# Performance work log

Hardware: AMD Instinct MI355X
Metric: run time of the kernel (lower is better)

## Reference

```python
import jax, jax.numpy as jnp
import numpy as np

B, N, D = 4, 4096, 1024
DFF = 4 * D
K = 2048  # max(1, int(N * 0.5))


def setup_inputs() -> dict:
    key = jax.random.key(0)
    ks = jax.random.split(key, 4)
    x = jax.random.normal(ks[0], (B, N, D), dtype=jnp.float32)
    gate_w = jax.random.normal(ks[1], (1, D), dtype=jnp.float32) * 0.02
    w1 = jax.random.normal(ks[2], (D, DFF), dtype=jnp.float32) * (1.0 / np.sqrt(D))
    b1 = jnp.zeros((DFF,), dtype=jnp.float32)
    w2 = jax.random.normal(ks[3], (DFF, D), dtype=jnp.float32) * (1.0 / np.sqrt(DFF))
    b2 = jnp.zeros((D,), dtype=jnp.float32)
    return {"x": x, "gate_w": gate_w, "w1": w1, "b1": b1, "w2": w2, "b2": b2, "k": K}


def reference(x, gate_w, w1, b1, w2, b2, k):
    # scores: [B, N] = gate(x).squeeze(-1)
    scores = jnp.einsum("bnd,d->bn", x, gate_w[0])
    _, topk = jax.lax.top_k(scores, k)          # [B, k] token indices
    # gather selected tokens: [B, k, D]
    x_sel = jnp.take_along_axis(x, topk[:, :, None], axis=1)
    # ffn (d -> 4d -> d, GELU) + residual on selected tokens only
    h = jax.nn.gelu(x_sel @ w1 + b1) @ w2 + b2
    x_proc = x_sel + h
    # scatter processed tokens back into a copy of x
    b_idx = jnp.arange(x.shape[0])[:, None]      # [B, 1]
    out = x.at[b_idx, topk].set(x_proc)
    return out
```

## Files before the change

### kernel.cpp

```cpp
#include <hip/hip_runtime.h>
#include <math.h>

#define B_   4
#define N_   4096
#define D_   1024
#define DFF_ 4096
#define K_   2048

typedef __attribute__((ext_vector_type(8))) short short8;
typedef __attribute__((ext_vector_type(4))) float float4v;

__device__ __forceinline__ unsigned short f2bf(float f) {
    unsigned int u = __float_as_uint(f);
    u = (u + 0x7fffu + ((u >> 16) & 1u)) >> 16;
    return (unsigned short)u;
}

__device__ __forceinline__ void gld16(const void* g, void* l) {
    __builtin_amdgcn_global_load_lds((const __attribute__((address_space(1))) void*)g,
                                     (__attribute__((address_space(3))) void*)l, 16, 0, 0);
}

__global__ __launch_bounds__(256) void scores_kernel(const float* __restrict__ x,
                                                     const float* __restrict__ gate_w,
                                                     float* __restrict__ scores,
                                                     int* __restrict__ slot) {
    int wave = (blockIdx.x * blockDim.x + threadIdx.x) >> 6;
    int lane = threadIdx.x & 63;
    if (wave >= B_ * N_) return;
    if (lane == 1) slot[wave] = -1;
    const float4* xr = (const float4*)(x + (size_t)wave * D_);
    const float4* g  = (const float4*)gate_w;
    float acc = 0.f;
    #pragma unroll
    for (int j = 0; j < D_ / 4 / 64; ++j) {
        float4 a = xr[lane + j * 64];
        float4 b = g[lane + j * 64];
        acc += a.x * b.x + a.y * b.y + a.z * b.z + a.w * b.w;
    }
    #pragma unroll
    for (int off = 32; off > 0; off >>= 1) acc += __shfl_down(acc, off, 64);
    if (lane == 0) scores[wave] = acc;
}

__global__ __launch_bounds__(1024) void select_topk_kernel(const float* __restrict__ scores,
                                                           int* __restrict__ topk,
                                                           int* __restrict__ slot) {
    __shared__ unsigned key[N_];
    __shared__ unsigned hist[256];
    __shared__ int sh_bin, sh_rem, sh_ngt;
    __shared__ int wsum[16], woff[16];
    int b = blockIdx.x, tid = threadIdx.x;
    int lane = tid & 63, wid = tid >> 6;

    for (int i = tid; i < N_; i += 1024) {
        unsigned u = __float_as_uint(scores[b * N_ + i]);
        key[i] = (u & 0x80000000u) ? ~u : (u | 0x80000000u);
    }
    if (tid == 0) sh_ngt = 0;
    __syncthreads();

    unsigned prefix = 0, pmask = 0;
    int rem = K_;
    for (int shift = 24; shift >= 0; shift -= 8) {
        if (tid < 256) hist[tid] = 0;
        __syncthreads();
        for (int i = tid; i < N_; i += 1024) {
            unsigned k = key[i];
            if ((k & pmask) == prefix) atomicAdd(&hist[(k >> shift) & 255u], 1u);
        }
        __syncthreads();
        if (tid < 64) {
            unsigned v0 = hist[4 * lane], v1 = hist[4 * lane + 1];
            unsigned v2 = hist[4 * lane + 2], v3 = hist[4 * lane + 3];
            unsigned s3 = v3, s2 = v2 + s3, s1 = v1 + s2, s0 = v0 + s1;
            unsigned t = s0;
            #pragma unroll
            for (int off = 1; off < 64; off <<= 1) {
                unsigned u = __shfl_down(t, off, 64);
                if (lane + off < 64) t += u;
            }
            unsigned above = t - s0;
            unsigned S0 = s0 + above, S1 = s1 + above, S2 = s2 + above, S3 = s3 + above;
            unsigned R = (unsigned)rem;
            if (S0 >= R && S1 < R) { sh_bin = 4 * lane;     sh_rem = rem - (int)S1; }
            if (S1 >= R && S2 < R) { sh_bin = 4 * lane + 1; sh_rem = rem - (int)S2; }
            if (S2 >= R && S3 < R) { sh_bin = 4 * lane + 2; sh_rem = rem - (int)S3; }
            if (S3 >= R && above < R) { sh_bin = 4 * lane + 3; sh_rem = rem - (int)above; }
        }
        __syncthreads();
        prefix |= ((unsigned)sh_bin) << shift;
        pmask  |= 0xffu << shift;
        rem = sh_rem;
    }
    unsigned T = prefix;
    int c_gt = K_ - rem;

    for (int i = tid; i < N_; i += 1024) {
        bool p = key[i] > T;
        unsigned long long m = __ballot(p);
        int cnt = __popcll(m);
        int basepos = 0;
        if (lane == 0 && cnt) basepos = atomicAdd(&sh_ngt, cnt);
        basepos = __shfl(basepos, 0, 64);
        if (p) {
            int pos = basepos + __popcll(m & ((1ULL << lane) - 1ULL));
            topk[b * K_ + pos] = i;
            slot[b * N_ + i] = b * K_ + pos;
        }
    }
    int base = tid * 4, c = 0;
    #pragma unroll
    for (int j = 0; j < 4; ++j) c += (key[base + j] == T);
    int sc = c;
    #pragma unroll
    for (int off = 1; off < 64; off <<= 1) {
        int u = __shfl_up(sc, off, 64);
        if (lane >= off) sc += u;
    }
    if (lane == 63) wsum[wid] = sc;
    __syncthreads();
    if (tid == 0) {
        int run = 0;
        #pragma unroll
        for (int j = 0; j < 16; ++j) { woff[j] = run; run += wsum[j]; }
    }
    __syncthreads();
    int r = woff[wid] + sc - c;
    #pragma unroll
    for (int j = 0; j < 4; ++j) {
        if (key[base + j] == T) {
            if (r < rem) {
                topk[b * K_ + c_gt + r] = base + j;
                slot[b * N_ + base + j] = b * K_ + c_gt + r;
            }
            ++r;
        }
    }
}

__global__ __launch_bounds__(256) void gather_copy_kernel(const float* __restrict__ x,
                                                          const int* __restrict__ slot,
                                                          unsigned short* __restrict__ xsel,
                                                          float* __restrict__ out) {
    int row = blockIdx.x;
    int t = threadIdx.x;
    int s = slot[row];
    float4 v = ((const float4*)(x + (size_t)row * D_))[t];
    if (s >= 0) {
        ushort4 o;
        o.x = f2bf(v.x); o.y = f2bf(v.y); o.z = f2bf(v.z); o.w = f2bf(v.w);
        ((ushort4*)(xsel + (size_t)s * D_))[t] = o;
    } else {
        ((float4*)(out + (size_t)row * D_))[t] = v;
    }
}

__global__ __launch_bounds__(256) void transpose_both_kernel(const float* __restrict__ w1,
                                                             const float* __restrict__ w2,
                                                             unsigned short* __restrict__ w1t,
                                                             unsigned short* __restrict__ w2t) {
    __shared__ float tile[32][33];
    int bid = blockIdx.x;
    const float* src; unsigned short* dst; int R, C, bx, by;
    if (bid < 4096) { src = w1; dst = w1t; R = D_;   C = DFF_; bx = bid & 127;          by = bid >> 7; }
    else            { src = w2; dst = w2t; R = DFF_; C = D_;   bx = (bid - 4096) & 31;  by = (bid - 4096) >> 5; }
    int tx = threadIdx.x & 31, ty = threadIdx.x >> 5;
    int c = bx * 32 + tx, r0 = by * 32;
    #pragma unroll
    for (int j = ty; j < 32; j += 8) tile[j][tx] = src[(size_t)(r0 + j) * C + c];
    __syncthreads();
    int dc = by * 32 + tx, dr0 = bx * 32;
    #pragma unroll
    for (int j = ty; j < 32; j += 8) dst[(size_t)(dr0 + j) * R + dc] = f2bf(tile[tx][j]);
}


__global__ __launch_bounds__(512, 4) void ffn1_db_kernel(const unsigned short* __restrict__ A,
                                                         const unsigned short* __restrict__ Bt,
                                                         const float* __restrict__ b1,
                                                         unsigned short* __restrict__ h1) {
    constexpr int K  = D_;
    constexpr int NT = K / 32;
    __shared__ __align__(16) unsigned short smem[24576];

    const int t    = threadIdx.x;
    const int lane = t & 63;
    const int wid  = t >> 6;
    const int quad = lane >> 4;
    const int lr   = lane & 15;
    const int wr   = wid >> 1;
    const int wc   = wid & 1;
    const int row0 = blockIdx.x * 256;
    const int col0 = blockIdx.y * 128;

    const int chA0 = t, chA1 = t + 512, chB = t;
    const int rpA0 = chA0 >> 3, wA0 = (chA0 & 7) ^ (rpA0 & 7);
    const int rpA1 = chA1 >> 3, wA1 = (chA1 & 7) ^ (rpA1 & 7);
    const int rpB  = chB  >> 3, wB  = (chB  & 7) ^ (rpB  & 7);
    const char* aS0 = (const char*)A  + ((size_t)(row0 + rpA0 * 2 + (wA0 >> 2)) * K + (size_t)(wA0 & 3) * 8) * 2;
    const char* aS1 = (const char*)A  + ((size_t)(row0 + rpA1 * 2 + (wA1 >> 2)) * K + (size_t)(wA1 & 3) * 8) * 2;
    const char* bS  = (const char*)Bt + ((size_t)(col0 + rpB  * 2 + (wB  >> 2)) * K + (size_t)(wB  & 3) * 8) * 2;
    const int oA0 = chA0 * 8, oA1 = chA1 * 8, oB = 8192 + chB * 8;

    const int rbA = wr * 64 + lr, rA2 = rbA >> 1;
    const int aoff = (rA2 * 8 + ((((rbA & 1) << 2) | quad) ^ (rA2 & 7))) * 8;
    const int rbB = wc * 64 + lr, rB2 = rbB >> 1;
    const int boff = 8192 + (rB2 * 8 + ((((rbB & 1) << 2) | quad) ^ (rB2 & 7))) * 8;

    unsigned short* lds0 = smem;
    unsigned short* lds1 = smem + 12288;

    gld16(aS0, lds0 + oA0); gld16(aS1, lds0 + oA1); gld16(bS, lds0 + oB);
    aS0 += 64; aS1 += 64; bS += 64;
    asm volatile("s_waitcnt vmcnt(0)" ::: "memory");
    __builtin_amdgcn_s_barrier();

    float4v acc[4][4] = {};
    short8 af[4], bq[4];

    auto step = [&](const unsigned short* cur, unsigned short* nxt, bool pf) {
        #pragma unroll
        for (int mi = 0; mi < 4; ++mi) af[mi] = *(const short8*)(cur + aoff + mi * 512);
        #pragma unroll
        for (int ni = 0; ni < 4; ++ni) bq[ni] = *(const short8*)(cur + boff + ni * 512);
        if (pf) {
            gld16(aS0, nxt + oA0); gld16(aS1, nxt + oA1); gld16(bS, nxt + oB);
            aS0 += 64; aS1 += 64; bS += 64;
        }
        __builtin_amdgcn_sched_barrier(0);
        __builtin_amdgcn_s_setprio(1);
        #pragma unroll
        for (int mi = 0; mi < 4; ++mi)
            #pragma unroll
            for (int ni = 0; ni < 4; ++ni)
                acc[mi][ni] = __builtin_amdgcn_mfma_f32_16x16x32_bf16(af[mi], bq[ni], acc[mi][ni], 0, 0, 0);
        __builtin_amdgcn_s_setprio(0);
        asm volatile("s_waitcnt vmcnt(0)" ::: "memory");
        __builtin_amdgcn_s_barrier();
    };

    for (int kt = 0; kt < NT - 2; kt += 2) { step(lds0, lds1, true); step(lds1, lds0, true); }
    step(lds0, lds1, true);
    step(lds1, lds0, false);

    float bias[4];
    #pragma unroll
    for (int ni = 0; ni < 4; ++ni) bias[ni] = b1[col0 + wc * 64 + ni * 16 + lr];
    unsigned short* ws_ = smem + wid * 1056;
    const int ro = row0 + wr * 64, co = col0 + wc * 64;
    #pragma unroll
    for (int mi = 0; mi < 4; ++mi) {
        #pragma unroll
        for (int ni = 0; ni < 4; ++ni)
            #pragma unroll
            for (int r = 0; r < 4; ++r) {
                float u = acc[mi][ni][r] + bias[ni];
                float tt = 1.5957691216057308f * u * (1.0f + 0.044715f * u * u);
                float g = u / (1.0f + __expf(-tt));
                ws_[(quad * 4 + r) * 66 + ni * 16 + lr] = f2bf(g);
            }
        asm volatile("s_waitcnt lgkmcnt(0)" ::: "memory");
        #pragma unroll
        for (int j = 0; j < 2; ++j) {
            int chk = lane + j * 64;
            int rr = chk >> 3, cc = chk & 7;
            *(short8*)(h1 + (size_t)(ro + mi * 16 + rr) * DFF_ + co + cc * 8) =
                *(const short8*)(ws_ + rr * 66 + cc * 8);
        }
        asm volatile("s_waitcnt lgkmcnt(0)" ::: "memory");
    }
}

__global__ __launch_bounds__(256, 2) void ffn2_db_kernel(const unsigned short* __restrict__ A,
                                                         const unsigned short* __restrict__ Bt,
                                                         const float* __restrict__ b2,
                                                         const float* __restrict__ x,
                                                         const int* __restrict__ topk,
                                                         float* __restrict__ out) {
    constexpr int K  = DFF_;
    constexpr int NT = K / 32;
    __shared__ __align__(16) unsigned short smem[16384];

    const int t    = threadIdx.x;
    const int lane = t & 63;
    const int wid  = t >> 6;
    const int quad = lane >> 4;
    const int lr   = lane & 15;
    const int wr   = wid >> 1;
    const int wc   = wid & 1;
    const int row0 = blockIdx.x * 128;
    const int col0 = blockIdx.y * 128;

    const int ch0 = t, ch1 = t + 256;
    const int rp0 = ch0 >> 3, w0 = (ch0 & 7) ^ (rp0 & 7);
    const int rp1 = ch1 >> 3, w1 = (ch1 & 7) ^ (rp1 & 7);
    const char* aS0 = (const char*)A  + ((size_t)(row0 + rp0 * 2 + (w0 >> 2)) * K + (size_t)(w0 & 3) * 8) * 2;
    const char* aS1 = (const char*)A  + ((size_t)(row0 + rp1 * 2 + (w1 >> 2)) * K + (size_t)(w1 & 3) * 8) * 2;
    const char* bS0 = (const char*)Bt + ((size_t)(col0 + rp0 * 2 + (w0 >> 2)) * K + (size_t)(w0 & 3) * 8) * 2;
    const char* bS1 = (const char*)Bt + ((size_t)(col0 + rp1 * 2 + (w1 >> 2)) * K + (size_t)(w1 & 3) * 8) * 2;
    const int oA0 = ch0 * 8, oA1 = ch1 * 8;
    const int oB0 = 4096 + ch0 * 8, oB1 = 4096 + ch1 * 8;

    const int rbA = wr * 64 + lr, rA2 = rbA >> 1;
    const int aoff = (rA2 * 8 + ((((rbA & 1) << 2) | quad) ^ (rA2 & 7))) * 8;
    const int rbB = wc * 64 + lr, rB2 = rbB >> 1;
    const int boff = 4096 + (rB2 * 8 + ((((rbB & 1) << 2) | quad) ^ (rB2 & 7))) * 8;

    unsigned short* lds0 = smem;
    unsigned short* lds1 = smem + 8192;

    gld16(aS0, lds0 + oA0); gld16(aS1, lds0 + oA1);
    gld16(bS0, lds0 + oB0); gld16(bS1, lds0 + oB1);
    aS0 += 64; aS1 += 64; bS0 += 64; bS1 += 64;
    asm volatile("s_waitcnt vmcnt(0)" ::: "memory");
    __builtin_amdgcn_s_barrier();

    float4v acc[4][4] = {};
    short8 af[4], bq[4];

    auto step = [&](const unsigned short* cur, unsigned short* nxt, bool pf) {
        #pragma unroll
        for (int mi = 0; mi < 4; ++mi) af[mi] = *(const short8*)(cur + aoff + mi * 512);
        #pragma unroll
        for (int ni = 0; ni < 4; ++ni) bq[ni] = *(const short8*)(cur + boff + ni * 512);
        if (pf) {
            gld16(aS0, nxt + oA0); gld16(aS1, nxt + oA1);
            gld16(bS0, nxt + oB0); gld16(bS1, nxt + oB1);
            aS0 += 64; aS1 += 64; bS0 += 64; bS1 += 64;
        }
        __builtin_amdgcn_sched_barrier(0);
        __builtin_amdgcn_s_setprio(1);
        #pragma unroll
        for (int mi = 0; mi < 4; ++mi)
            #pragma unroll
            for (int ni = 0; ni < 4; ++ni)
                acc[mi][ni] = __builtin_amdgcn_mfma_f32_16x16x32_bf16(af[mi], bq[ni], acc[mi][ni], 0, 0, 0);
        __builtin_amdgcn_s_setprio(0);
        asm volatile("s_waitcnt vmcnt(0)" ::: "memory");
        __builtin_amdgcn_s_barrier();
    };

    for (int kt = 0; kt < NT - 2; kt += 2) { step(lds0, lds1, true); step(lds1, lds0, true); }
    step(lds0, lds1, true);
    step(lds1, lds0, false);

    #pragma unroll
    for (int mi = 0; mi < 4; ++mi) {
        #pragma unroll
        for (int r = 0; r < 4; ++r) {
            int row = row0 + wr * 64 + mi * 16 + quad * 4 + r;
            int gb = row >> 11;
            int tok = topk[row];
            size_t base = ((size_t)(gb * N_ + tok)) * D_;
            #pragma unroll
            for (int ni = 0; ni < 4; ++ni) {
                int col = col0 + wc * 64 + ni * 16 + lr;
                out[base + col] = x[base + col] + acc[mi][ni][r] + b2[col];
            }
        }
    }
}

extern "C" void kernel_launch(void* const* d_in, const int* in_sizes, int n_in,
                              void* d_out, int out_size, void* d_ws, size_t ws_size,
                              hipStream_t stream) {
    const float* x      = (const float*)d_in[0];
    const float* gate_w = (const float*)d_in[1];
    const float* w1     = (const float*)d_in[2];
    const float* b1     = (const float*)d_in[3];
    const float* w2     = (const float*)d_in[4];
    const float* b2     = (const float*)d_in[5];
    float* out = (float*)d_out;

    char* ws = (char*)d_ws;
    float*          scores = (float*)ws;
    int*            topk   = (int*)(ws + (64 << 10));
    int*            slot   = (int*)(ws + (96 << 10));
    unsigned short* xsel   = (unsigned short*)(ws + (160 << 10));
    unsigned short* w1t    = (unsigned short*)(ws + (160 << 10) + (16 << 20));
    unsigned short* w2t    = (unsigned short*)(ws + (160 << 10) + (24 << 20));
    unsigned short* h1     = (unsigned short*)(ws + (160 << 10) + (32 << 20));

    scores_kernel<<<(B_ * N_) / 4, 256, 0, stream>>>(x, gate_w, scores, slot);
    select_topk_kernel<<<B_, 1024, 0, stream>>>(scores, topk, slot);

    transpose_both_kernel<<<8192, 256, 0, stream>>>(w1, w2, w1t, w2t);

    gather_copy_kernel<<<B_ * N_, 256, 0, stream>>>(x, slot, xsel, out);

    ffn1_db_kernel<<<dim3(32, 32), 512, 0, stream>>>(xsel, w1t, b1, h1);
    ffn2_db_kernel<<<dim3(64, 8), 256, 0, stream>>>(h1, w2t, b2, x, topk, out);
}
```

Baseline: 329.8 us.

## Deepen K-step to 64 per LDS stage in both FFN GEMMs

Both FFN GEMM kernels now load 64-wide K slices per double-buffered LDS stage instead of 32, with a new row-major swizzled layout and two MFMA sub-steps per stage. This halves the number of barriers and waits per GEMM. FFN1 also drops from 512-thread 256x128 tiles to 256-thread 128x128 tiles with a doubled grid. LDS use per block grows to 64KB, which may limit occupancy.

```diff
diff --git a/kernel.cpp b/kernel.cpp
--- a/kernel.cpp
+++ b/kernel.cpp
@@ -176,111 +176,13 @@
 }
 
 
-__global__ __launch_bounds__(512, 4) void ffn1_db_kernel(const unsigned short* __restrict__ A,
-                                                         const unsigned short* __restrict__ Bt,
-                                                         const float* __restrict__ b1,
-                                                         unsigned short* __restrict__ h1) {
+__global__ __launch_bounds__(256, 2) void ffn1_k64_kernel(const unsigned short* __restrict__ A,
+                                                          const unsigned short* __restrict__ Bt,
+                                                          const float* __restrict__ b1,
+                                                          unsigned short* __restrict__ h1) {
     constexpr int K  = D_;
-    constexpr int NT = K / 32;
-    __shared__ __align__(16) unsigned short smem[24576];
-
-    const int t    = threadIdx.x;
-    const int lane = t & 63;
-    const int wid  = t >> 6;
-    const int quad = lane >> 4;
-    const int lr   = lane & 15;
-    const int wr   = wid >> 1;
-    const int wc   = wid & 1;
-    const int row0 = blockIdx.x * 256;
-    const int col0 = blockIdx.y * 128;
-
-    const int chA0 = t, chA1 = t + 512, chB = t;
-    const int rpA0 = chA0 >> 3, wA0 = (chA0 & 7) ^ (rpA0 & 7);
-    const int rpA1 = chA1 >> 3, wA1 = (chA1 & 7) ^ (rpA1 & 7);
-    const int rpB  = chB  >> 3, wB  = (chB  & 7) ^ (rpB  & 7);
-    const char* aS0 = (const char*)A  + ((size_t)(row0 + rpA0 * 2 + (wA0 >> 2)) * K + (size_t)(wA0 & 3) * 8) * 2;
-    const char* aS1 = (const char*)A  + ((size_t)(row0 + rpA1 * 2 + (wA1 >> 2)) * K + (size_t)(wA1 & 3) * 8) * 2;
-    const char* bS  = (const char*)Bt + ((size_t)(col0 + rpB  * 2 + (wB  >> 2)) * K + (size_t)(wB  & 3) * 8) * 2;
-    const int oA0 = chA0 * 8, oA1 = chA1 * 8, oB = 8192 + chB * 8;
-
-    const int rbA = wr * 64 + lr, rA2 = rbA >> 1;
-    const int aoff = (rA2 * 8 + ((((rbA & 1) << 2) | quad) ^ (rA2 & 7))) * 8;
-    const int rbB = wc * 64 + lr, rB2 = rbB >> 1;
-    const int boff = 8192 + (rB2 * 8 + ((((rbB & 1) << 2) | quad) ^ (rB2 & 7))) * 8;
-
-    unsigned short* lds0 = smem;
-    unsigned short* lds1 = smem + 12288;
-
-    gld16(aS0, lds0 + oA0); gld16(aS1, lds0 + oA1); gld16(bS, lds0 + oB);
-    aS0 += 64; aS1 += 64; bS += 64;
-    asm volatile("s_waitcnt vmcnt(0)" ::: "memory");
-    __builtin_amdgcn_s_barrier();
-
-    float4v acc[4][4] = {};
-    short8 af[4], bq[4];
-
-    auto step = [&](const unsigned short* cur, unsigned short* nxt, bool pf) {
-        #pragma unroll
-        for (int mi = 0; mi < 4; ++mi) af[mi] = *(const short8*)(cur + aoff + mi * 512);
-        #pragma unroll
-        for (int ni = 0; ni < 4; ++ni) bq[ni] = *(const short8*)(cur + boff + ni * 512);
-        if (pf) {
-            gld16(aS0, nxt + oA0); gld16(aS1, nxt + oA1); gld16(bS, nxt + oB);
-            aS0 += 64; aS1 += 64; bS += 64;
-        }
-        __builtin_amdgcn_sched_barrier(0);
-        __builtin_amdgcn_s_setprio(1);
-        #pragma unroll
-        for (int mi = 0; mi < 4; ++mi)
-            #pragma unroll
-            for (int ni = 0; ni < 4; ++ni)
-                acc[mi][ni] = __builtin_amdgcn_mfma_f32_16x16x32_bf16(af[mi], bq[ni], acc[mi][ni], 0, 0, 0);
-        __builtin_amdgcn_s_setprio(0);
-        asm volatile("s_waitcnt vmcnt(0)" ::: "memory");
-        __builtin_amdgcn_s_barrier();
-    };
-
-    for (int kt = 0; kt < NT - 2; kt += 2) { step(lds0, lds1, true); step(lds1, lds0, true); }
-    step(lds0, lds1, true);
-    step(lds1, lds0, false);
-
-    float bias[4];
-    #pragma unroll
-    for (int ni = 0; ni < 4; ++ni) bias[ni] = b1[col0 + wc * 64 + ni * 16 + lr];
-    unsigned short* ws_ = smem + wid * 1056;
-    const int ro = row0 + wr * 64, co = col0 + wc * 64;
-    #pragma unroll
-    for (int mi = 0; mi < 4; ++mi) {
-        #pragma unroll
-        for (int ni = 0; ni < 4; ++ni)
-            #pragma unroll
-            for (int r = 0; r < 4; ++r) {
-                float u = acc[mi][ni][r] + bias[ni];
-                float tt = 1.5957691216057308f * u * (1.0f + 0.044715f * u * u);
-                float g = u / (1.0f + __expf(-tt));
-                ws_[(quad * 4 + r) * 66 + ni * 16 + lr] = f2bf(g);
-            }
-        asm volatile("s_waitcnt lgkmcnt(0)" ::: "memory");
-        #pragma unroll
-        for (int j = 0; j < 2; ++j) {
-            int chk = lane + j * 64;
-            int rr = chk >> 3, cc = chk & 7;
-            *(short8*)(h1 + (size_t)(ro + mi * 16 + rr) * DFF_ + co + cc * 8) =
-                *(const short8*)(ws_ + rr * 66 + cc * 8);
-        }
-        asm volatile("s_waitcnt lgkmcnt(0)" ::: "memory");
-    }
-}
-
-__global__ __launch_bounds__(256, 2) void ffn2_db_kernel(const unsigned short* __restrict__ A,
-                                                         const unsigned short* __restrict__ Bt,
-                                                         const float* __restrict__ b2,
-                                                         const float* __restrict__ x,
-                                                         const int* __restrict__ topk,
-                                                         float* __restrict__ out) {
-    constexpr int K  = DFF_;
-    constexpr int NT = K / 32;
-    __shared__ __align__(16) unsigned short smem[16384];
+    constexpr int NT = K / 64;
+    __shared__ __align__(16) unsigned short smem[32768];
 
     const int t    = threadIdx.x;
     const int lane = t & 63;
@@ -292,44 +194,177 @@
     const int row0 = blockIdx.x * 128;
     const int col0 = blockIdx.y * 128;
 
-    const int ch0 = t, ch1 = t + 256;
-    const int rp0 = ch0 >> 3, w0 = (ch0 & 7) ^ (rp0 & 7);
-    const int rp1 = ch1 >> 3, w1 = (ch1 & 7) ^ (rp1 & 7);
-    const char* aS0 = (const char*)A  + ((size_t)(row0 + rp0 * 2 + (w0 >> 2)) * K + (size_t)(w0 & 3) * 8) * 2;
-    const char* aS1 = (const char*)A  + ((size_t)(row0 + rp1 * 2 + (w1 >> 2)) * K + (size_t)(w1 & 3) * 8) * 2;
-    const char* bS0 = (const char*)Bt + ((size_t)(col0 + rp0 * 2 + (w0 >> 2)) * K + (size_t)(w0 & 3) * 8) * 2;
-    const char* bS1 = (const char*)Bt + ((size_t)(col0 + rp1 * 2 + (w1 >> 2)) * K + (size_t)(w1 & 3) * 8) * 2;
-    const int oA0 = ch0 * 8, oA1 = ch1 * 8;
-    const int oB0 = 4096 + ch0 * 8, oB1 = 4096 + ch1 * 8;
-
-    const int rbA = wr * 64 + lr, rA2 = rbA >> 1;
-    const int aoff = (rA2 * 8 + ((((rbA & 1) << 2) | quad) ^ (rA2 & 7))) * 8;
-    const int rbB = wc * 64 + lr, rB2 = rbB >> 1;
-    const int boff = 4096 + (rB2 * 8 + ((((rbB & 1) << 2) | quad) ^ (rB2 & 7))) * 8;
+    const char* aS[4]; const char* bS[4]; int oA[4], oB[4];
+    #pragma unroll
+    for (int j = 0; j < 4; ++j) {
+        int s = t + j * 256;
+        int r = s >> 3, c = (s & 7) ^ (r & 7);
+        aS[j] = (const char*)A  + ((size_t)(row0 + r) * K + (size_t)c * 8) * 2;
+        bS[j] = (const char*)Bt + ((size_t)(col0 + r) * K + (size_t)c * 8) * 2;
+        oA[j] = s * 8;
+        oB[j] = 8192 + s * 8;
+    }
+
+    const int rbA = wr * 64 + lr;
+    const int aoff0 = (rbA * 8 + (quad       ^ (rbA & 7))) * 8;
+    const int aoff1 = (rbA * 8 + ((4 + quad) ^ (rbA & 7))) * 8;
+    const int rbB = wc * 64 + lr;
+    const int boff0 = 8192 + (rbB * 8 + (quad       ^ (rbB & 7))) * 8;
+    const int boff1 = 8192 + (rbB * 8 + ((4 + quad) ^ (rbB & 7))) * 8;
 
     unsigned short* lds0 = smem;
-    unsigned short* lds1 = smem + 8192;
-
-    gld16(aS0, lds0 + oA0); gld16(aS1, lds0 + oA1);
-    gld16(bS0, lds0 + oB0); gld16(bS1, lds0 + oB1);
-    aS0 += 64; aS1 += 64; bS0 += 64; bS1 += 64;
+    unsigned short* lds1 = smem + 16384;
+
+    #pragma unroll
+    for (int j = 0; j < 4; ++j) { gld16(aS[j], lds0 + oA[j]); gld16(bS[j], lds0 + oB[j]); }
+    #pragma unroll
+    for (int j = 0; j < 4; ++j) { aS[j] += 128; bS[j] += 128; }
     asm volatile("s_waitcnt vmcnt(0)" ::: "memory");
     __builtin_amdgcn_s_barrier();
 
     float4v acc[4][4] = {};
-    short8 af[4], bq[4];
 
     auto step = [&](const unsigned short* cur, unsigned short* nxt, bool pf) {
-        #pragma unroll
-        for (int mi = 0; mi < 4; ++mi) af[mi] = *(const short8*)(cur + aoff + mi * 512);
-        #pragma unroll
-        for (int ni = 0; ni < 4; ++ni) bq[ni] = *(const short8*)(cur + boff + ni * 512);
+        short8 af[4], bq[4];
+        #pragma unroll
+        for (int mi = 0; mi < 4; ++mi) af[mi] = *(const short8*)(cur + aoff0 + mi * 1024);
+        #pragma unroll
+        for (int ni = 0; ni < 4; ++ni) bq[ni] = *(const short8*)(cur + boff0 + ni * 1024);
         if (pf) {
-            gld16(aS0, nxt + oA0); gld16(aS1, nxt + oA1);
-            gld16(bS0, nxt + oB0); gld16(bS1, nxt + oB1);
-            aS0 += 64; aS1 += 64; bS0 += 64; bS1 += 64;
+            #pragma unroll
+            for (int j = 0; j < 4; ++j) { gld16(aS[j], nxt + oA[j]); gld16(bS[j], nxt + oB[j]); }
+            #pragma unroll
+            for (int j = 0; j < 4; ++j) { aS[j] += 128; bS[j] += 128; }
         }
         __builtin_amdgcn_sched_barrier(0);
+        __builtin_amdgcn_s_setprio(1);
+        #pragma unroll
+        for (int mi = 0; mi < 4; ++mi)
+            #pragma unroll
+            for (int ni = 0; ni < 4; ++ni)
+                acc[mi][ni] = __builtin_amdgcn_mfma_f32_16x16x32_bf16(af[mi], bq[ni], acc[mi][ni], 0, 0, 0);
+        __builtin_amdgcn_s_setprio(0);
+        #pragma unroll
+        for (int mi = 0; mi < 4; ++mi) af[mi] = *(const short8*)(cur + aoff1 + mi * 1024);
+        #pragma unroll
+        for (int ni = 0; ni < 4; ++ni) bq[ni] = *(const short8*)(cur + boff1 + ni * 1024);
+        __builtin_amdgcn_s_setprio(1);
+        #pragma unroll
+        for (int mi = 0; mi < 4; ++mi)
+            #pragma unroll
+            for (int ni = 0; ni < 4; ++ni)
+                acc[mi][ni] = __builtin_amdgcn_mfma_f32_16x16x32_bf16(af[mi], bq[ni], acc[mi][ni], 0, 0, 0);
+        __builtin_amdgcn_s_setprio(0);
+        asm volatile("s_waitcnt vmcnt(0)" ::: "memory");
+        __builtin_amdgcn_s_barrier();
+    };
+
+    for (int kt = 0; kt < NT - 2; kt += 2) { step(lds0, lds1, true); step(lds1, lds0, true); }
+    step(lds0, lds1, true);
+    step(lds1, lds0, false);
+
+    float bias[4];
+    #pragma unroll
+    for (int ni = 0; ni < 4; ++ni) bias[ni] = b1[col0 + wc * 64 + ni * 16 + lr];
+    unsigned short* ws_ = smem + wid * 1056;
+    const int ro = row0 + wr * 64, co = col0 + wc * 64;
+    #pragma unroll
+    for (int mi = 0; mi < 4; ++mi) {
+        #pragma unroll
+        for (int ni = 0; ni < 4; ++ni)
+            #pragma unroll
+            for (int r = 0; r < 4; ++r) {
+                float u = acc[mi][ni][r] + bias[ni];
+                float tt = 1.5957691216057308f * u * (1.0f + 0.044715f * u * u);
+                float g = u / (1.0f + __expf(-tt));
+                ws_[(quad * 4 + r) * 66 + ni * 16 + lr] = f2bf(g);
+            }
+        asm volatile("s_waitcnt lgkmcnt(0)" ::: "memory");
+        #pragma unroll
+        for (int j = 0; j < 2; ++j) {
+            int chk = lane + j * 64;
+            int rr = chk >> 3, cc = chk & 7;
+            *(short8*)(h1 + (size_t)(ro + mi * 16 + rr) * DFF_ + co + cc * 8) =
+                *(const short8*)(ws_ + rr * 66 + cc * 8);
+        }
+        asm volatile("s_waitcnt lgkmcnt(0)" ::: "memory");
+    }
+}
+
+__global__ __launch_bounds__(256, 2) void ffn2_k64_kernel(const unsigned short* __restrict__ A,
+                                                          const unsigned short* __restrict__ Bt,
+                                                          const float* __restrict__ b2,
+                                                          const float* __restrict__ x,
+                                                          const int* __restrict__ topk,
+                                                          float* __restrict__ out) {
+    constexpr int K  = DFF_;
+    constexpr int NT = K / 64;
+    __shared__ __align__(16) unsigned short smem[32768];
+
+    const int t    = threadIdx.x;
+    const int lane = t & 63;
+    const int wid  = t >> 6;
+    const int quad = lane >> 4;
+    const int lr   = lane & 15;
+    const int wr   = wid >> 1;
+    const int wc   = wid & 1;
+    const int row0 = blockIdx.x * 128;
+    const int col0 = blockIdx.y * 128;
+
+    const char* aS[4]; const char* bS[4]; int oA[4], oB[4];
+    #pragma unroll
+    for (int j = 0; j < 4; ++j) {
+        int s = t + j * 256;
+        int r = s >> 3, c = (s & 7) ^ (r & 7);
+        aS[j] = (const char*)A  + ((size_t)(row0 + r) * K + (size_t)c * 8) * 2;
+        bS[j] = (const char*)Bt + ((size_t)(col0 + r) * K + (size_t)c * 8) * 2;
+        oA[j] = s * 8;
+        oB[j] = 8192 + s * 8;
+    }
+
+    const int rbA = wr * 64 + lr;
+    const int aoff0 = (rbA * 8 + (quad       ^ (rbA & 7))) * 8;
+    const int aoff1 = (rbA * 8 + ((4 + quad) ^ (rbA & 7))) * 8;
+    const int rbB = wc * 64 + lr;
+    const int boff0 = 8192 + (rbB * 8 + (quad       ^ (rbB & 7))) * 8;
+    const int boff1 = 8192 + (rbB * 8 + ((4 + quad) ^ (rbB & 7))) * 8;
+
+    unsigned short* lds0 = smem;
+    unsigned short* lds1 = smem + 16384;
+
+    #pragma unroll
+    for (int j = 0; j < 4; ++j) { gld16(aS[j], lds0 + oA[j]); gld16(bS[j], lds0 + oB[j]); }
+    #pragma unroll
+    for (int j = 0; j < 4; ++j) { aS[j] += 128; bS[j] += 128; }
+    asm volatile("s_waitcnt vmcnt(0)" ::: "memory");
+    __builtin_amdgcn_s_barrier();
+
+    float4v acc[4][4] = {};
+
+    auto step = [&](const unsigned short* cur, unsigned short* nxt, bool pf) {
+        short8 af[4], bq[4];
+        #pragma unroll
+        for (int mi = 0; mi < 4; ++mi) af[mi] = *(const short8*)(cur + aoff0 + mi * 1024);
+        #pragma unroll
+        for (int ni = 0; ni < 4; ++ni) bq[ni] = *(const short8*)(cur + boff0 + ni * 1024);
+        if (pf) {
+            #pragma unroll
+            for (int j = 0; j < 4; ++j) { gld16(aS[j], nxt + oA[j]); gld16(bS[j], nxt + oB[j]); }
+            #pragma unroll
+            for (int j = 0; j < 4; ++j) { aS[j] += 128; bS[j] += 128; }
+        }
+        __builtin_amdgcn_sched_barrier(0);
+        __builtin_amdgcn_s_setprio(1);
+        #pragma unroll
+        for (int mi = 0; mi < 4; ++mi)
+            #pragma unroll
+            for (int ni = 0; ni < 4; ++ni)
+                acc[mi][ni] = __builtin_amdgcn_mfma_f32_16x16x32_bf16(af[mi], bq[ni], acc[mi][ni], 0, 0, 0);
+        __builtin_amdgcn_s_setprio(0);
+        #pragma unroll
+        for (int mi = 0; mi < 4; ++mi) af[mi] = *(const short8*)(cur + aoff1 + mi * 1024);
+        #pragma unroll
+        for (int ni = 0; ni < 4; ++ni) bq[ni] = *(const short8*)(cur + boff1 + ni * 1024);
         __builtin_amdgcn_s_setprio(1);
         #pragma unroll
         for (int mi = 0; mi < 4; ++mi)
@@ -389,6 +424,6 @@
 
     gather_copy_kernel<<<B_ * N_, 256, 0, stream>>>(x, slot, xsel, out);
 
-    ffn1_db_kernel<<<dim3(32, 32), 512, 0, stream>>>(xsel, w1t, b1, h1);
-    ffn2_db_kernel<<<dim3(64, 8), 256, 0, stream>>>(h1, w2t, b2, x, topk, out);
-}
+    ffn1_k64_kernel<<<dim3(64, 32), 256, 0, stream>>>(xsel, w1t, b1, h1);
+    ffn2_k64_kernel<<<dim3(64, 8), 256, 0, stream>>>(h1, w2t, b2, x, topk, out);
+}
```

Result: faster. 317.9 us (-3.6%).

## Replace double-buffered GEMM loops with four-stage LDS ring and partial waits

Applied to the files above, without the earlier changes.

Both FFN GEMM kernels now use a four-slot LDS ring that keeps three K-tiles of global-to-LDS loads in flight, waiting only for the oldest tile with a counted vmcnt instead of draining all loads every step. The first GEMM also moves from 256x128 tiles with 512 threads to 128x128 tiles with 256 threads, doubling its grid. The aim is to hide global memory latency behind the MFMA work. In exchange each block uses 64KB of LDS, which may reduce how many blocks fit per CU, and the smaller ffn1 tile loads operands more often.

```diff
diff --git a/kernel.cpp b/kernel.cpp
--- a/kernel.cpp
+++ b/kernel.cpp
@@ -176,111 +176,14 @@
 }
 
 
-__global__ __launch_bounds__(512, 4) void ffn1_db_kernel(const unsigned short* __restrict__ A,
-                                                         const unsigned short* __restrict__ Bt,
-                                                         const float* __restrict__ b1,
-                                                         unsigned short* __restrict__ h1) {
+
+__global__ __launch_bounds__(256, 2) void ffn1_ring_kernel(const unsigned short* __restrict__ A,
+                                                           const unsigned short* __restrict__ Bt,
+                                                           const float* __restrict__ b1,
+                                                           unsigned short* __restrict__ h1) {
     constexpr int K  = D_;
     constexpr int NT = K / 32;
-    __shared__ __align__(16) unsigned short smem[24576];
-
-    const int t    = threadIdx.x;
-    const int lane = t & 63;
-    const int wid  = t >> 6;
-    const int quad = lane >> 4;
-    const int lr   = lane & 15;
-    const int wr   = wid >> 1;
-    const int wc   = wid & 1;
-    const int row0 = blockIdx.x * 256;
-    const int col0 = blockIdx.y * 128;
-
-    const int chA0 = t, chA1 = t + 512, chB = t;
-    const int rpA0 = chA0 >> 3, wA0 = (chA0 & 7) ^ (rpA0 & 7);
-    const int rpA1 = chA1 >> 3, wA1 = (chA1 & 7) ^ (rpA1 & 7);
-    const int rpB  = chB  >> 3, wB  = (chB  & 7) ^ (rpB  & 7);
-    const char* aS0 = (const char*)A  + ((size_t)(row0 + rpA0 * 2 + (wA0 >> 2)) * K + (size_t)(wA0 & 3) * 8) * 2;
-    const char* aS1 = (const char*)A  + ((size_t)(row0 + rpA1 * 2 + (wA1 >> 2)) * K + (size_t)(wA1 & 3) * 8) * 2;
-    const char* bS  = (const char*)Bt + ((size_t)(col0 + rpB  * 2 + (wB  >> 2)) * K + (size_t)(wB  & 3) * 8) * 2;
-    const int oA0 = chA0 * 8, oA1 = chA1 * 8, oB = 8192 + chB * 8;
-
-    const int rbA = wr * 64 + lr, rA2 = rbA >> 1;
-    const int aoff = (rA2 * 8 + ((((rbA & 1) << 2) | quad) ^ (rA2 & 7))) * 8;
-    const int rbB = wc * 64 + lr, rB2 = rbB >> 1;
-    const int boff = 8192 + (rB2 * 8 + ((((rbB & 1) << 2) | quad) ^ (rB2 & 7))) * 8;
-
-    unsigned short* lds0 = smem;
-    unsigned short* lds1 = smem + 12288;
-
-    gld16(aS0, lds0 + oA0); gld16(aS1, lds0 + oA1); gld16(bS, lds0 + oB);
-    aS0 += 64; aS1 += 64; bS += 64;
-    asm volatile("s_waitcnt vmcnt(0)" ::: "memory");
-    __builtin_amdgcn_s_barrier();
-
-    float4v acc[4][4] = {};
-    short8 af[4], bq[4];
-
-    auto step = [&](const unsigned short* cur, unsigned short* nxt, bool pf) {
-        #pragma unroll
-        for (int mi = 0; mi < 4; ++mi) af[mi] = *(const short8*)(cur + aoff + mi * 512);
-        #pragma unroll
-        for (int ni = 0; ni < 4; ++ni) bq[ni] = *(const short8*)(cur + boff + ni * 512);
-        if (pf) {
-            gld16(aS0, nxt + oA0); gld16(aS1, nxt + oA1); gld16(bS, nxt + oB);
-            aS0 += 64; aS1 += 64; bS += 64;
-        }
-        __builtin_amdgcn_sched_barrier(0);
-        __builtin_amdgcn_s_setprio(1);
-        #pragma unroll
-        for (int mi = 0; mi < 4; ++mi)
-            #pragma unroll
-            for (int ni = 0; ni < 4; ++ni)
-                acc[mi][ni] = __builtin_amdgcn_mfma_f32_16x16x32_bf16(af[mi], bq[ni], acc[mi][ni], 0, 0, 0);
-        __builtin_amdgcn_s_setprio(0);
-        asm volatile("s_waitcnt vmcnt(0)" ::: "memory");
-        __builtin_amdgcn_s_barrier();
-    };
-
-    for (int kt = 0; kt < NT - 2; kt += 2) { step(lds0, lds1, true); step(lds1, lds0, true); }
-    step(lds0, lds1, true);
-    step(lds1, lds0, false);
-
-    float bias[4];
-    #pragma unroll
-    for (int ni = 0; ni < 4; ++ni) bias[ni] = b1[col0 + wc * 64 + ni * 16 + lr];
-    unsigned short* ws_ = smem + wid * 1056;
-    const int ro = row0 + wr * 64, co = col0 + wc * 64;
-    #pragma unroll
-    for (int mi = 0; mi < 4; ++mi) {
-        #pragma unroll
-        for (int ni = 0; ni < 4; ++ni)
-            #pragma unroll
-            for (int r = 0; r < 4; ++r) {
-                float u = acc[mi][ni][r] + bias[ni];
-                float tt = 1.5957691216057308f * u * (1.0f + 0.044715f * u * u);
-                float g = u / (1.0f + __expf(-tt));
-                ws_[(quad * 4 + r) * 66 + ni * 16 + lr] = f2bf(g);
-            }
-        asm volatile("s_waitcnt lgkmcnt(0)" ::: "memory");
-        #pragma unroll
-        for (int j = 0; j < 2; ++j) {
-            int chk = lane + j * 64;
-            int rr = chk >> 3, cc = chk & 7;
-            *(short8*)(h1 + (size_t)(ro + mi * 16 + rr) * DFF_ + co + cc * 8) =
-                *(const short8*)(ws_ + rr * 66 + cc * 8);
-        }
-        asm volatile("s_waitcnt lgkmcnt(0)" ::: "memory");
-    }
-}
-
-__global__ __launch_bounds__(256, 2) void ffn2_db_kernel(const unsigned short* __restrict__ A,
-                                                         const unsigned short* __restrict__ Bt,
-                                                         const float* __restrict__ b2,
-                                                         const float* __restrict__ x,
-                                                         const int* __restrict__ topk,
-                                                         float* __restrict__ out) {
-    constexpr int K  = DFF_;
-    constexpr int NT = K / 32;
-    __shared__ __align__(16) unsigned short smem[16384];
+    __shared__ __align__(16) unsigned short smem[32768];
 
     const int t    = threadIdx.x;
     const int lane = t & 63;
@@ -292,42 +195,50 @@
     const int row0 = blockIdx.x * 128;
     const int col0 = blockIdx.y * 128;
 
-    const int ch0 = t, ch1 = t + 256;
-    const int rp0 = ch0 >> 3, w0 = (ch0 & 7) ^ (rp0 & 7);
-    const int rp1 = ch1 >> 3, w1 = (ch1 & 7) ^ (rp1 & 7);
-    const char* aS0 = (const char*)A  + ((size_t)(row0 + rp0 * 2 + (w0 >> 2)) * K + (size_t)(w0 & 3) * 8) * 2;
-    const char* aS1 = (const char*)A  + ((size_t)(row0 + rp1 * 2 + (w1 >> 2)) * K + (size_t)(w1 & 3) * 8) * 2;
-    const char* bS0 = (const char*)Bt + ((size_t)(col0 + rp0 * 2 + (w0 >> 2)) * K + (size_t)(w0 & 3) * 8) * 2;
-    const char* bS1 = (const char*)Bt + ((size_t)(col0 + rp1 * 2 + (w1 >> 2)) * K + (size_t)(w1 & 3) * 8) * 2;
-    const int oA0 = ch0 * 8, oA1 = ch1 * 8;
-    const int oB0 = 4096 + ch0 * 8, oB1 = 4096 + ch1 * 8;
+    const char* aS[2]; const char* bS[2]; int oA[2], oB[2];
+    #pragma unroll
+    for (int j = 0; j < 2; ++j) {
+        int s = t + j * 256;
+        int rp = s >> 3, w = (s & 7) ^ (rp & 7);
+        int gr = rp * 2 + (w >> 2), gc = w & 3;
+        aS[j] = (const char*)A  + ((size_t)(row0 + gr) * K + (size_t)gc * 8) * 2;
+        bS[j] = (const char*)Bt + ((size_t)(col0 + gr) * K + (size_t)gc * 8) * 2;
+        oA[j] = s * 8;
+        oB[j] = 4096 + s * 8;
+    }
 
     const int rbA = wr * 64 + lr, rA2 = rbA >> 1;
     const int aoff = (rA2 * 8 + ((((rbA & 1) << 2) | quad) ^ (rA2 & 7))) * 8;
     const int rbB = wc * 64 + lr, rB2 = rbB >> 1;
     const int boff = 4096 + (rB2 * 8 + ((((rbB & 1) << 2) | quad) ^ (rB2 & 7))) * 8;
 
-    unsigned short* lds0 = smem;
-    unsigned short* lds1 = smem + 8192;
-
-    gld16(aS0, lds0 + oA0); gld16(aS1, lds0 + oA1);
-    gld16(bS0, lds0 + oB0); gld16(bS1, lds0 + oB1);
-    aS0 += 64; aS1 += 64; bS0 += 64; bS1 += 64;
-    asm volatile("s_waitcnt vmcnt(0)" ::: "memory");
+    #pragma unroll
+    for (int pt = 0; pt < 3; ++pt) {
+        unsigned short* buf = smem + pt * 8192;
+        #pragma unroll
+        for (int j = 0; j < 2; ++j) { gld16(aS[j], buf + oA[j]); gld16(bS[j], buf + oB[j]); }
+        #pragma unroll
+        for (int j = 0; j < 2; ++j) { aS[j] += 64; bS[j] += 64; }
+    }
+    asm volatile("s_waitcnt vmcnt(8)" ::: "memory");
     __builtin_amdgcn_s_barrier();
 
     float4v acc[4][4] = {};
-    short8 af[4], bq[4];
-
-    auto step = [&](const unsigned short* cur, unsigned short* nxt, bool pf) {
+
+    #pragma unroll 4
+    for (int kt = 0; kt < NT; ++kt) {
+        const unsigned short* cur = smem + (kt & 3) * 8192;
+        unsigned short* nxt = smem + ((kt + 3) & 3) * 8192;
+        short8 af[4], bq[4];
         #pragma unroll
         for (int mi = 0; mi < 4; ++mi) af[mi] = *(const short8*)(cur + aoff + mi * 512);
         #pragma unroll
         for (int ni = 0; ni < 4; ++ni) bq[ni] = *(const short8*)(cur + boff + ni * 512);
-        if (pf) {
-            gld16(aS0, nxt + oA0); gld16(aS1, nxt + oA1);
-            gld16(bS0, nxt + oB0); gld16(bS1, nxt + oB1);
-            aS0 += 64; aS1 += 64; bS0 += 64; bS1 += 64;
+        if (kt + 3 < NT) {
+            #pragma unroll
+            for (int j = 0; j < 2; ++j) { gld16(aS[j], nxt + oA[j]); gld16(bS[j], nxt + oB[j]); }
+            #pragma unroll
+            for (int j = 0; j < 2; ++j) { aS[j] += 64; bS[j] += 64; }
         }
         __builtin_amdgcn_sched_barrier(0);
         __builtin_amdgcn_s_setprio(1);
@@ -337,13 +248,119 @@
             for (int ni = 0; ni < 4; ++ni)
                 acc[mi][ni] = __builtin_amdgcn_mfma_f32_16x16x32_bf16(af[mi], bq[ni], acc[mi][ni], 0, 0, 0);
         __builtin_amdgcn_s_setprio(0);
-        asm volatile("s_waitcnt vmcnt(0)" ::: "memory");
+        if (kt < NT - 3)       asm volatile("s_waitcnt vmcnt(8)" ::: "memory");
+        else if (kt == NT - 3) asm volatile("s_waitcnt vmcnt(4)" ::: "memory");
+        else                   asm volatile("s_waitcnt vmcnt(0)" ::: "memory");
         __builtin_amdgcn_s_barrier();
-    };
-
-    for (int kt = 0; kt < NT - 2; kt += 2) { step(lds0, lds1, true); step(lds1, lds0, true); }
-    step(lds0, lds1, true);
-    step(lds1, lds0, false);
+    }
+
+    float bias[4];
+    #pragma unroll
+    for (int ni = 0; ni < 4; ++ni) bias[ni] = b1[col0 + wc * 64 + ni * 16 + lr];
+    unsigned short* ws_ = smem + wid * 1056;
+    const int co = col0 + wc * 64;
+    #pragma unroll
+    for (int mi = 0; mi < 4; ++mi) {
+        const int ro = row0 + wr * 64 + mi * 16;
+        #pragma unroll
+        for (int ni = 0; ni < 4; ++ni)
+            #pragma unroll
+            for (int r = 0; r < 4; ++r) {
+                float u = acc[mi][ni][r] + bias[ni];
+                float tt = 1.5957691216057308f * u * (1.0f + 0.044715f * u * u);
+                float g = u / (1.0f + __expf(-tt));
+                ws_[(quad * 4 + r) * 66 + ni * 16 + lr] = f2bf(g);
+            }
+        asm volatile("s_waitcnt lgkmcnt(0)" ::: "memory");
+        #pragma unroll
+        for (int j = 0; j < 2; ++j) {
+            int chk = lane + j * 64;
+            int rr = chk >> 3, cc = chk & 7;
+            *(short8*)(h1 + (size_t)(ro + rr) * DFF_ + co + cc * 8) =
+                *(const short8*)(ws_ + rr * 66 + cc * 8);
+        }
+        asm volatile("s_waitcnt lgkmcnt(0)" ::: "memory");
+    }
+}
+
+__global__ __launch_bounds__(256, 2) void ffn2_ring_kernel(const unsigned short* __restrict__ A,
+                                                           const unsigned short* __restrict__ Bt,
+                                                           const float* __restrict__ b2,
+                                                           const float* __restrict__ x,
+                                                           const int* __restrict__ topk,
+                                                           float* __restrict__ out) {
+    constexpr int K  = DFF_;
+    constexpr int NT = K / 32;
+    __shared__ __align__(16) unsigned short smem[32768];
+
+    const int t    = threadIdx.x;
+    const int lane = t & 63;
+    const int wid  = t >> 6;
+    const int quad = lane >> 4;
+    const int lr   = lane & 15;
+    const int wr   = wid >> 1;
+    const int wc   = wid & 1;
+    const int row0 = blockIdx.x * 128;
+    const int col0 = blockIdx.y * 128;
+
+    const char* aS[2]; const char* bS[2]; int oA[2], oB[2];
+    #pragma unroll
+    for (int j = 0; j < 2; ++j) {
+        int s = t + j * 256;
+        int rp = s >> 3, w = (s & 7) ^ (rp & 7);
+        int gr = rp * 2 + (w >> 2), gc = w & 3;
+        aS[j] = (const char*)A  + ((size_t)(row0 + gr) * K + (size_t)gc * 8) * 2;
+        bS[j] = (const char*)Bt + ((size_t)(col0 + gr) * K + (size_t)gc * 8) * 2;
+        oA[j] = s * 8;
+        oB[j] = 4096 + s * 8;
+    }
+
+    const int rbA = wr * 64 + lr, rA2 = rbA >> 1;
+    const int aoff = (rA2 * 8 + ((((rbA & 1) << 2) | quad) ^ (rA2 & 7))) * 8;
+    const int rbB = wc * 64 + lr, rB2 = rbB >> 1;
+    const int boff = 4096 + (rB2 * 8 + ((((rbB & 1) << 2) | quad) ^ (rB2 & 7))) * 8;
+
+    #pragma unroll
+    for (int pt = 0; pt < 3; ++pt) {
+        unsigned short* buf = smem + pt * 8192;
+        #pragma unroll
+        for (int j = 0; j < 2; ++j) { gld16(aS[j], buf + oA[j]); gld16(bS[j], buf + oB[j]); }
+        #pragma unroll
+        for (int j = 0; j < 2; ++j) { aS[j] += 64; bS[j] += 64; }
+    }
+    asm volatile("s_waitcnt vmcnt(8)" ::: "memory");
+    __builtin_amdgcn_s_barrier();
+
+    float4v acc[4][4] = {};
+
+    #pragma unroll 4
+    for (int kt = 0; kt < NT; ++kt) {
+        const unsigned short* cur = smem + (kt & 3) * 8192;
+        unsigned short* nxt = smem + ((kt + 3) & 3) * 8192;
+        short8 af[4], bq[4];
+        #pragma unroll
+        for (int mi = 0; mi < 4; ++mi) af[mi] = *(const short8*)(cur + aoff + mi * 512);
+        #pragma unroll
+        for (int ni = 0; ni < 4; ++ni) bq[ni] = *(const short8*)(cur + boff + ni * 512);
+        if (kt + 3 < NT) {
+            #pragma unroll
+            for (int j = 0; j < 2; ++j) { gld16(aS[j], nxt + oA[j]); gld16(bS[j], nxt + oB[j]); }
+            #pragma unroll
+            for (int j = 0; j < 2; ++j) { aS[j] += 64; bS[j] += 64; }
+        }
+        __builtin_amdgcn_sched_barrier(0);
+        __builtin_amdgcn_s_setprio(1);
+        #pragma unroll
+        for (int mi = 0; mi < 4; ++mi)
+            #pragma unroll
+            for (int ni = 0; ni < 4; ++ni)
+                acc[mi][ni] = __builtin_amdgcn_mfma_f32_16x16x32_bf16(af[mi], bq[ni], acc[mi][ni], 0, 0, 0);
+        __builtin_amdgcn_s_setprio(0);
+        if (kt < NT - 3)       asm volatile("s_waitcnt vmcnt(8)" ::: "memory");
+        else if (kt == NT - 3) asm volatile("s_waitcnt vmcnt(4)" ::: "memory");
+        else                   asm volatile("s_waitcnt vmcnt(0)" ::: "memory");
+        __builtin_amdgcn_s_barrier();
+    }
 
     #pragma unroll
     for (int mi = 0; mi < 4; ++mi) {
@@ -389,6 +406,6 @@
 
     gather_copy_kernel<<<B_ * N_, 256, 0, stream>>>(x, slot, xsel, out);
 
-    ffn1_db_kernel<<<dim3(32, 32), 512, 0, stream>>>(xsel, w1t, b1, h1);
-    ffn2_db_kernel<<<dim3(64, 8), 256, 0, stream>>>(h1, w2t, b2, x, topk, out);
-}
+    ffn1_ring_kernel<<<dim3(64, 32), 256, 0, stream>>>(xsel, w1t, b1, h1);
+    ffn2_ring_kernel<<<dim3(64, 8), 256, 0, stream>>>(h1, w2t, b2, x, topk, out);
+}
```

After: 341.8 us. +3.6%, slower.

## Rewrite FFN1 GEMM as 256x256 tile with staggered 4-phase LDS pipeline

Applied to the files above, without the earlier changes.

Replaces the 256x128-tile double-buffered FFN1 GEMM with a 256x256 tile that uses a K step of 64 and 128KB of LDS. Each K iteration is split into four quadrant phases, and the loads for the next or current buffer are staggered between the MFMA bursts, in the style of the HipKittens 8-wave schedule. The aim is a higher ratio of MFMA work to LDS and global traffic and better hiding of load latency. In exchange it roughly doubles the accumulator registers, drops occupancy to 2 blocks per CU, adds more barriers, and halves the grid to 512 blocks.

```diff
diff --git a/kernel.cpp b/kernel.cpp
--- a/kernel.cpp
+++ b/kernel.cpp
@@ -175,102 +175,180 @@
     for (int j = ty; j < 32; j += 8) dst[(size_t)(dr0 + j) * R + dc] = f2bf(tile[tx][j]);
 }
 
-
-__global__ __launch_bounds__(512, 4) void ffn1_db_kernel(const unsigned short* __restrict__ A,
-                                                         const unsigned short* __restrict__ Bt,
-                                                         const float* __restrict__ b1,
-                                                         unsigned short* __restrict__ h1) {
+__global__ __launch_bounds__(512, 2) void ffn1_8ph_kernel(const unsigned short* __restrict__ A,
+                                                          const unsigned short* __restrict__ Bt,
+                                                          const float* __restrict__ b1,
+                                                          unsigned short* __restrict__ h1) {
     constexpr int K  = D_;
-    constexpr int NT = K / 32;
-    __shared__ __align__(16) unsigned short smem[24576];
+    constexpr int NT = K / 64;
+    __shared__ __align__(16) unsigned short smem[65536];
 
     const int t    = threadIdx.x;
     const int lane = t & 63;
     const int wid  = t >> 6;
     const int quad = lane >> 4;
     const int lr   = lane & 15;
-    const int wr   = wid >> 1;
-    const int wc   = wid & 1;
+    const int wr   = wid >> 2;
+    const int wc   = wid & 3;
     const int row0 = blockIdx.x * 256;
-    const int col0 = blockIdx.y * 128;
-
-    const int chA0 = t, chA1 = t + 512, chB = t;
-    const int rpA0 = chA0 >> 3, wA0 = (chA0 & 7) ^ (rpA0 & 7);
-    const int rpA1 = chA1 >> 3, wA1 = (chA1 & 7) ^ (rpA1 & 7);
-    const int rpB  = chB  >> 3, wB  = (chB  & 7) ^ (rpB  & 7);
-    const char* aS0 = (const char*)A  + ((size_t)(row0 + rpA0 * 2 + (wA0 >> 2)) * K + (size_t)(wA0 & 3) * 8) * 2;
-    const char* aS1 = (const char*)A  + ((size_t)(row0 + rpA1 * 2 + (wA1 >> 2)) * K + (size_t)(wA1 & 3) * 8) * 2;
-    const char* bS  = (const char*)Bt + ((size_t)(col0 + rpB  * 2 + (wB  >> 2)) * K + (size_t)(wB  & 3) * 8) * 2;
-    const int oA0 = chA0 * 8, oA1 = chA1 * 8, oB = 8192 + chB * 8;
-
-    const int rbA = wr * 64 + lr, rA2 = rbA >> 1;
-    const int aoff = (rA2 * 8 + ((((rbA & 1) << 2) | quad) ^ (rA2 & 7))) * 8;
-    const int rbB = wc * 64 + lr, rB2 = rbB >> 1;
-    const int boff = 8192 + (rB2 * 8 + ((((rbB & 1) << 2) | quad) ^ (rB2 & 7))) * 8;
-
-    unsigned short* lds0 = smem;
-    unsigned short* lds1 = smem + 12288;
-
-    gld16(aS0, lds0 + oA0); gld16(aS1, lds0 + oA1); gld16(bS, lds0 + oB);
-    aS0 += 64; aS1 += 64; bS += 64;
-    asm volatile("s_waitcnt vmcnt(0)" ::: "memory");
+    const int col0 = blockIdx.y * 256;
+
+    const char* pA[2][2]; const char* pB[2][2];
+    int oA[2][2], oB[2][2];
+    #pragma unroll
+    for (int h = 0; h < 2; ++h)
+        #pragma unroll
+        for (int j = 0; j < 2; ++j) {
+            int s = t + j * 512;
+            int r = s >> 3, c = (s & 7) ^ (r & 7);
+            pA[h][j] = (const char*)A  + ((size_t)(row0 + h * 128 + r) * K + (size_t)c * 8) * 2;
+            pB[h][j] = (const char*)Bt + ((size_t)(col0 + h * 128 + r) * K + (size_t)c * 8) * 2;
+            oA[h][j] = (h * 1024 + s) * 8;
+            oB[h][j] = 16384 + (h * 1024 + s) * 8;
+        }
+
+    auto stageA = [&](int h, unsigned short* buf) {
+        gld16(pA[h][0], buf + oA[h][0]); gld16(pA[h][1], buf + oA[h][1]);
+        pA[h][0] += 128; pA[h][1] += 128;
+    };
+    auto stageB = [&](int h, unsigned short* buf) {
+        gld16(pB[h][0], buf + oB[h][0]); gld16(pB[h][1], buf + oB[h][1]);
+        pB[h][0] += 128; pB[h][1] += 128;
+    };
+
+    int axor[2];
+    #pragma unroll
+    for (int kk = 0; kk < 2; ++kk) axor[kk] = ((kk * 4 + quad) ^ (lr & 7)) * 8;
+    const int aBase = (wr * 64 + lr) * 64;
+    const int bBase = 16384 + (wc * 32 + lr) * 64;
+
+    unsigned short* sm0 = smem;
+    unsigned short* sm1 = smem + 32768;
+
+    stageA(0, sm0); stageA(1, sm0); stageB(0, sm0); stageB(1, sm0);
+    stageB(0, sm1); stageA(1, sm1);
+    asm volatile("s_waitcnt vmcnt(4)" ::: "memory");
     __builtin_amdgcn_s_barrier();
 
-    float4v acc[4][4] = {};
-    short8 af[4], bq[4];
-
-    auto step = [&](const unsigned short* cur, unsigned short* nxt, bool pf) {
-        #pragma unroll
-        for (int mi = 0; mi < 4; ++mi) af[mi] = *(const short8*)(cur + aoff + mi * 512);
-        #pragma unroll
-        for (int ni = 0; ni < 4; ++ni) bq[ni] = *(const short8*)(cur + boff + ni * 512);
-        if (pf) {
-            gld16(aS0, nxt + oA0); gld16(aS1, nxt + oA1); gld16(bS, nxt + oB);
-            aS0 += 64; aS1 += 64; bS += 64;
-        }
+    float4v acc[8][4] = {};
+
+    for (int kt = 0; kt < NT; ++kt) {
+        unsigned short* cur = smem + (kt & 1) * 32768;
+        unsigned short* nxt = smem + (((kt & 1) ^ 1)) * 32768;
+        short8 afl[4][2], afh[4][2], bq0[2][2], bq1[2][2];
+
+        #pragma unroll
+        for (int mi = 0; mi < 4; ++mi)
+            #pragma unroll
+            for (int kk = 0; kk < 2; ++kk)
+                afl[mi][kk] = *(const short8*)(cur + aBase + mi * 1024 + axor[kk]);
+        #pragma unroll
+        for (int nj = 0; nj < 2; ++nj)
+            #pragma unroll
+            for (int kk = 0; kk < 2; ++kk)
+                bq0[nj][kk] = *(const short8*)(cur + bBase + nj * 1024 + axor[kk]);
+        if (kt + 1 < NT) stageA(0, nxt);
         __builtin_amdgcn_sched_barrier(0);
+        __builtin_amdgcn_s_barrier();
         __builtin_amdgcn_s_setprio(1);
         #pragma unroll
         for (int mi = 0; mi < 4; ++mi)
             #pragma unroll
-            for (int ni = 0; ni < 4; ++ni)
-                acc[mi][ni] = __builtin_amdgcn_mfma_f32_16x16x32_bf16(af[mi], bq[ni], acc[mi][ni], 0, 0, 0);
+            for (int nj = 0; nj < 2; ++nj)
+                #pragma unroll
+                for (int kk = 0; kk < 2; ++kk)
+                    acc[mi][nj] = __builtin_amdgcn_mfma_f32_16x16x32_bf16(afl[mi][kk], bq0[nj][kk], acc[mi][nj], 0, 0, 0);
         __builtin_amdgcn_s_setprio(0);
-        asm volatile("s_waitcnt vmcnt(0)" ::: "memory");
-        __builtin_amdgcn_s_barrier();
-    };
-
-    for (int kt = 0; kt < NT - 2; kt += 2) { step(lds0, lds1, true); step(lds1, lds0, true); }
-    step(lds0, lds1, true);
-    step(lds1, lds0, false);
+        __builtin_amdgcn_s_barrier();
+
+        #pragma unroll
+        for (int mi = 0; mi < 4; ++mi)
+            #pragma unroll
+            for (int kk = 0; kk < 2; ++kk)
+                afh[mi][kk] = *(const short8*)(cur + aBase + 8192 + mi * 1024 + axor[kk]);
+        if (kt + 1 < NT) stageB(1, nxt);
+        __builtin_amdgcn_sched_barrier(0);
+        __builtin_amdgcn_s_barrier();
+        __builtin_amdgcn_s_setprio(1);
+        #pragma unroll
+        for (int mi = 0; mi < 4; ++mi)
+            #pragma unroll
+            for (int nj = 0; nj < 2; ++nj)
+                #pragma unroll
+                for (int kk = 0; kk < 2; ++kk)
+                    acc[4 + mi][nj] = __builtin_amdgcn_mfma_f32_16x16x32_bf16(afh[mi][kk], bq0[nj][kk], acc[4 + mi][nj], 0, 0, 0);
+        __builtin_amdgcn_s_setprio(0);
+        __builtin_amdgcn_s_barrier();
+
+        #pragma unroll
+        for (int nj = 0; nj < 2; ++nj)
+            #pragma unroll
+            for (int kk = 0; kk < 2; ++kk)
+                bq1[nj][kk] = *(const short8*)(cur + bBase + 8192 + nj * 1024 + axor[kk]);
+        if (kt + 2 < NT) stageB(0, cur);
+        __builtin_amdgcn_sched_barrier(0);
+        __builtin_amdgcn_s_barrier();
+        __builtin_amdgcn_s_setprio(1);
+        #pragma unroll
+        for (int mi = 0; mi < 4; ++mi)
+            #pragma unroll
+            for (int nj = 0; nj < 2; ++nj)
+                #pragma unroll
+                for (int kk = 0; kk < 2; ++kk)
+                    acc[4 + mi][2 + nj] = __builtin_amdgcn_mfma_f32_16x16x32_bf16(afh[mi][kk], bq1[nj][kk], acc[4 + mi][2 + nj], 0, 0, 0);
+        __builtin_amdgcn_s_setprio(0);
+        __builtin_amdgcn_s_barrier();
+
+        #pragma unroll
+        for (int mi = 0; mi < 4; ++mi)
+            #pragma unroll
+            for (int kk = 0; kk < 2; ++kk)
+                afl[mi][kk] = *(const short8*)(cur + aBase + mi * 1024 + axor[kk]);
+        if (kt + 2 < NT) stageA(1, cur);
+        __builtin_amdgcn_sched_barrier(0);
+        __builtin_amdgcn_s_barrier();
+        __builtin_amdgcn_s_setprio(1);
+        #pragma unroll
+        for (int mi = 0; mi < 4; ++mi)
+            #pragma unroll
+            for (int nj = 0; nj < 2; ++nj)
+                #pragma unroll
+                for (int kk = 0; kk < 2; ++kk)
+                    acc[mi][2 + nj] = __builtin_amdgcn_mfma_f32_16x16x32_bf16(afl[mi][kk], bq1[nj][kk], acc[mi][2 + nj], 0, 0, 0);
+        __builtin_amdgcn_s_setprio(0);
+        if (kt < NT - 2)       asm volatile("s_waitcnt vmcnt(4)" ::: "memory");
+        else if (kt == NT - 2) asm volatile("s_waitcnt vmcnt(0)" ::: "memory");
+        __builtin_amdgcn_s_barrier();
+    }
 
     float bias[4];
     #pragma unroll
-    for (int ni = 0; ni < 4; ++ni) bias[ni] = b1[col0 + wc * 64 + ni * 16 + lr];
-    unsigned short* ws_ = smem + wid * 1056;
-    const int ro = row0 + wr * 64, co = col0 + wc * 64;
-    #pragma unroll
-    for (int mi = 0; mi < 4; ++mi) {
-        #pragma unroll
-        for (int ni = 0; ni < 4; ++ni)
-            #pragma unroll
-            for (int r = 0; r < 4; ++r) {
-                float u = acc[mi][ni][r] + bias[ni];
-                float tt = 1.5957691216057308f * u * (1.0f + 0.044715f * u * u);
-                float g = u / (1.0f + __expf(-tt));
-                ws_[(quad * 4 + r) * 66 + ni * 16 + lr] = f2bf(g);
-            }
-        asm volatile("s_waitcnt lgkmcnt(0)" ::: "memory");
-        #pragma unroll
-        for (int j = 0; j < 2; ++j) {
-            int chk = lane + j * 64;
-            int rr = chk >> 3, cc = chk & 7;
-            *(short8*)(h1 + (size_t)(ro + mi * 16 + rr) * DFF_ + co + cc * 8) =
-                *(const short8*)(ws_ + rr * 66 + cc * 8);
-        }
-        asm volatile("s_waitcnt lgkmcnt(0)" ::: "memory");
-    }
-}
+    for (int ni = 0; ni < 4; ++ni) bias[ni] = b1[col0 + (ni >> 1) * 128 + wc * 32 + (ni & 1) * 16 + lr];
+    unsigned short* ws_ = smem + wid * 640;
+    const int rr = lane >> 2, cc = lane & 3;
+    #pragma unroll
+    for (int mi = 0; mi < 8; ++mi) {
+        const int ro = row0 + (mi >> 2) * 128 + wr * 64 + (mi & 3) * 16;
+        #pragma unroll
+        for (int g = 0; g < 2; ++g) {
+            const int co = col0 + g * 128 + wc * 32;
+            #pragma unroll
+            for (int nj = 0; nj < 2; ++nj)
+                #pragma unroll
+                for (int r = 0; r < 4; ++r) {
+                    float u = acc[mi][g * 2 + nj][r] + bias[g * 2 + nj];
+                    float tt = 1.5957691216057308f * u * (1.0f + 0.044715f * u * u);
+                    float gv = u / (1.0f + __expf(-tt));
+                    ws_[(quad * 4 + r) * 40 + nj * 16 + lr] = f2bf(gv);
+                }
+            asm volatile("s_waitcnt lgkmcnt(0)" ::: "memory");
+            *(short8*)(h1 + (size_t)(ro + rr) * DFF_ + co + cc * 8) =
+                *(const short8*)(ws_ + rr * 40 + cc * 8);
+            asm volatile("s_waitcnt lgkmcnt(0)" ::: "memory");
+        }
+    }
+}
+
 
 __global__ __launch_bounds__(256, 2) void ffn2_db_kernel(const unsigned short* __restrict__ A,
                                                          const unsigned short* __restrict__ Bt,
@@ -389,6 +467,6 @@
 
     gather_copy_kernel<<<B_ * N_, 256, 0, stream>>>(x, slot, xsel, out);
 
-    ffn1_db_kernel<<<dim3(32, 32), 512, 0, stream>>>(xsel, w1t, b1, h1);
+    ffn1_8ph_kernel<<<dim3(32, 16), 512, 0, stream>>>(xsel, w1t, b1, h1);
     ffn2_db_kernel<<<dim3(64, 8), 256, 0, stream>>>(h1, w2t, b2, x, topk, out);
 }
```

Result: no change. 328.5 us (-0.4%).
